# Kernel tuning notes

Measured on AMD Instinct MI355X. Metric: run time of the kernel, lower is better.

The kernel has to match this reference:

```python
import jax, jax.numpy as jnp
import numpy as np

EPS = 1e-8
NU_MOLECULAR = 1.5e-05
# loss weights (module defaults)
DATA_W, BC_W, TURB_W, RANS_W, SMOOTH_W, WALL_W = 1.0, 0.05, 0.05, 0.05, 0.01, 0.02
CONT_INIT = CONT_TGT = 0.1
MOM_INIT = MOM_TGT = 0.1
RAMP_STEPS, RAMP_START = 1000, 0

N_NODES, N_EDGES = 100000, 6400000


def _curriculum_weights(step):
    if step < RAMP_START:
        return CONT_INIT, MOM_INIT
    if step >= RAMP_START + RAMP_STEPS:
        return CONT_TGT, MOM_TGT
    alpha = (step - RAMP_START) / RAMP_STEPS  # linear ramp
    return ((1 - alpha) * CONT_INIT + alpha * CONT_TGT,
            (1 - alpha) * MOM_INIT + alpha * MOM_TGT)


def setup_inputs() -> dict:
    key = jax.random.key(0)
    k1, k2, k3, k4, k5 = jax.random.split(key, 5)
    predictions = jax.random.normal(k1, (N_NODES, 4), dtype=jnp.float32)
    targets = jax.random.normal(k2, (N_NODES, 4), dtype=jnp.float32)
    # dx, dy strictly positive edge offsets
    edge_attr_dxdy = jax.random.uniform(k3, (N_EDGES, 2), dtype=jnp.float32, minval=1e-3, maxval=0.05)
    edge_index = jax.random.randint(k4, (2, N_EDGES), 0, N_NODES, dtype=jnp.int64)
    wall_mask = jax.random.bernoulli(k5, 0.05, (N_NODES,))
    return {"predictions": predictions, "targets": targets,
            "edge_attr_dxdy": edge_attr_dxdy, "edge_index": edge_index,
            "wall_mask": wall_mask, "step": 500}


def reference(predictions, targets, edge_attr_dxdy, edge_index, wall_mask, step):
    cont_w, mom_w = _curriculum_weights(int(step))
    N = predictions.shape[0]
    row, col = edge_index[0], edge_index[1]
    u, v, p, nu_t = (predictions[:, i] for i in range(4))
    dx, dy = edge_attr_dxdy[:, 0], edge_attr_dxdy[:, 1]

    # per-edge finite differences (single gather of node fields)
    du = u[col] - u[row]
    dv = v[col] - v[row]
    dp = p[col] - p[row]

    seg = lambda e: jax.ops.segment_sum(e, row, num_segments=N)
    edge_count = jnp.maximum(seg(jnp.ones_like(du)), 1.0)

    # --- data loss ---
    mse_loss = jnp.mean((predictions - targets) ** 2)

    # --- continuity (divergence) loss ---
    divergence = (seg(du / (dx + EPS)) + seg(dv / (dy + EPS))) / edge_count
    div_loss = jnp.mean(divergence ** 2)

    # --- momentum loss ---
    p_grad_x = seg(dp / (dx + EPS)) / edge_count
    p_grad_y = seg(dp / (dy + EPS)) / edge_count
    lap_u = seg(du / (dx ** 2 + EPS)) / edge_count
    lap_v = seg(dv / (dy ** 2 + EPS)) / edge_count
    nu_eff = NU_MOLECULAR + nu_t
    momentum_loss = jnp.mean((p_grad_x + nu_eff * lap_u) ** 2 +
                             (p_grad_y + nu_eff * lap_v) ** 2)

    # --- turbulence losses ---
    positivity_loss = jnp.mean(jax.nn.relu(-nu_t) ** 2)
    du_dx = du / (dx + EPS)
    du_dy = du / (dy + EPS)
    dv_dx = dv / (dx + EPS)
    dv_dy = dv / (dy + EPS)
    strain_sq_edge = 2.0 * (du_dx ** 2 + dv_dy ** 2) + (du_dy + dv_dx) ** 2
    strain_node = seg(strain_sq_edge) / edge_count
    production = nu_t * strain_node
    turb_production_loss = jnp.mean(production ** 2)
    turb_dissipation_loss = jnp.mean(nu_t ** 2)

    # --- boundary-condition & wall-function losses (wall mask) ---
    m = wall_mask.astype(u.dtype)
    n_wall = jnp.maximum(jnp.sum(m), 1.0)
    bc_loss = jnp.sum(m * (u ** 2 + v ** 2)) / n_wall
    wall_loss = jnp.sum(m * (u ** 2 + v ** 2 + nu_t ** 2)) / n_wall

    # --- smoothness loss over edges ---
    smooth_loss = jnp.mean((predictions[col] - predictions[row]) ** 2)

    total = (DATA_W * mse_loss + cont_w * div_loss + mom_w * momentum_loss +
             TURB_W * turb_production_loss + RANS_W * turb_dissipation_loss +
             BC_W * bc_loss + SMOOTH_W * smooth_loss + WALL_W * wall_loss)
    # positivity_loss is tracked but not weighted into total (per visible code paths)
    return total
```

## Files before the change

### kernel.cpp

```cpp
#include <hip/hip_runtime.h>
#include <hip/hip_fp16.h>

#define EPS 1e-8f
#define NU_MOL 1.5e-5f
#define NPB 512
#define MAXNB 256
#define NBP 256
#define NBLK 2048
#define CMAX 3328
#define KMAX 13
#define HB 7
#define CH 1536
#define KACC 3
#define SPLIT 6
#define NGRP 32
#define GRP 64


union U32H2 { unsigned u; __half2 h; };

__device__ inline unsigned packh2(float a, float b) {
    U32H2 x; x.h = __halves2half2(__float2half_rn(a), __float2half_rn(b));
    return x.u;
}
__device__ inline float2 unpackh2(unsigned u) {
    U32H2 x; x.u = u;
    return make_float2(__low2float(x.h), __high2float(x.h));
}

__device__ inline int detect64(const void* eidx, int N) {
    const long long* ll = (const long long*)eidx;
    int is64 = 1;
    #pragma unroll
    for (int i = 0; i < 16; ++i) {
        long long v = ll[i];
        if (v < 0 || v >= (long long)N) is64 = 0;
    }
    return is64;
}


__global__ void detect_idx_dtype(const void* eidx, int N, int* flag) {
    const long long* ll = (const long long*)eidx;
    int is64 = 1;
    for (int i = 0; i < 16; ++i) {
        long long v = ll[i];
        if (v < 0 || v >= (long long)N) { is64 = 0; break; }
    }
    *flag = is64;
}

__global__ void finalize_kernel(const double* __restrict__ d,
                                const double* __restrict__ smooth_slots,
                                int N, int E, float* __restrict__ out)
{
    double smooth = 0.0;
    for (int i = 0; i < 64; ++i) smooth += smooth_slots[i];
    double dN = (double)N;
    double n_wall = d[5] > 1.0 ? d[5] : 1.0;
    double total = 1.0  * d[0] / (4.0 * dN)
                 + 0.1  * d[1] / dN
                 + 0.1  * d[2] / dN
                 + 0.05 * d[3] / dN
                 + 0.05 * d[4] / dN
                 + 0.05 * d[6] / n_wall
                 + 0.01 * smooth / (4.0 * (double)E)
                 + 0.02 * d[7] / n_wall;
    out[0] = (float)total;
}


__global__ __launch_bounds__(256) void count_kernel(
    const void* __restrict__ eidx, int E, int N, int NB,
    unsigned* __restrict__ counts, unsigned* __restrict__ gsum)
{
    __shared__ unsigned hist[4][MAXNB];
    hist[0][threadIdx.x] = 0u;
    hist[1][threadIdx.x] = 0u;
    hist[2][threadIdx.x] = 0u;
    hist[3][threadIdx.x] = 0u;
    __syncthreads();
    const int w = (threadIdx.x >> 6) & 3;
    const int is64 = detect64(eidx, N);
    const long long* ll = (const long long*)eidx;
    const int* ii = (const int*)eidx;
    int chunk = (E + NBLK - 1) / NBLK;
    int s = blockIdx.x * chunk;
    int Cb = min(chunk, E - s);

    unsigned rr[KMAX];
    #pragma unroll
    for (int k = 0; k < KMAX; ++k) {
        int i = k * 256 + threadIdx.x;
        if (i < Cb) {
            int r = is64 ? (int)ll[s + i] : ii[s + i];
            rr[k] = (unsigned)min(max(r, 0), N - 1);
        } else rr[k] = 0xFFFFFFFFu;
    }
    #pragma unroll
    for (int k = 0; k < KMAX; ++k)
        if (rr[k] != 0xFFFFFFFFu)
            atomicAdd(&hist[w][rr[k] >> 9], 1u);
    __syncthreads();
    if (threadIdx.x < NB) {
        unsigned h = hist[0][threadIdx.x] + hist[1][threadIdx.x]
                   + hist[2][threadIdx.x] + hist[3][threadIdx.x];
        counts[(size_t)blockIdx.x * NBP + threadIdx.x] = h;
        if (h) atomicAdd(&gsum[(size_t)(blockIdx.x >> 6) * NBP + threadIdx.x], h);
    }
}

__global__ __launch_bounds__(512) void scan_base_kernel(
    unsigned* __restrict__ gsum, unsigned* __restrict__ base, int NB)
{
    __shared__ unsigned sc[512];
    int t = threadIdx.x;
    unsigned vg[NGRP];
    unsigned total = 0;
    if (t < NB) {
        #pragma unroll
        for (int g = 0; g < NGRP; ++g) {
            vg[g] = gsum[(size_t)g * NBP + t];
            total += vg[g];
        }
    }
    sc[t] = total; __syncthreads();
    for (int off = 1; off < 512; off <<= 1) {
        unsigned x = (t >= off) ? sc[t - off] : 0u;
        __syncthreads();
        sc[t] += x;
        __syncthreads();
    }
    unsigned ex = sc[t] - total;
    if (t < NB) {
        base[t] = ex;
        unsigned run = ex;
        #pragma unroll
        for (int g = 0; g < NGRP; ++g) {
            unsigned x = vg[g];
            gsum[(size_t)g * NBP + t] = run;
            run += x;
        }
    }
    if (t == 511) base[NB] = sc[511];
}

__global__ __launch_bounds__(256) void local_scan_kernel(
    unsigned* __restrict__ counts, const unsigned* __restrict__ gsum, int NB)
{
    __shared__ unsigned segs[4][64];
    int g = blockIdx.x;
    int b0 = blockIdx.y * 64;
    int j = threadIdx.x & 63, seg = threadIdx.x >> 6;
    int b = b0 + j;
    unsigned v[16];
    unsigned ssum = 0;
    if (b < NB) {
        #pragma unroll
        for (int k = 0; k < 16; ++k) {
            int row = g * GRP + seg * 16 + k;
            v[k] = counts[(size_t)row * NBP + b];
            ssum += v[k];
        }
    }
    segs[seg][j] = ssum;
    __syncthreads();
    if (b < NB) {
        unsigned carry = gsum[(size_t)g * NBP + b];
        for (int s_ = 0; s_ < seg; ++s_) carry += segs[s_][j];
        #pragma unroll
        for (int k = 0; k < 16; ++k) {
            int row = g * GRP + seg * 16 + k;
            counts[(size_t)row * NBP + b] = carry;
            carry += v[k];
        }
    }
}

__global__ __launch_bounds__(256) void scatter_kernel(
    const void* __restrict__ eidx, const float2* __restrict__ eattr,
    int E, int N, int NB,
    const unsigned* __restrict__ localoff ,
    uint2* __restrict__ vals)
{
    __shared__ unsigned hist[2][MAXNB];
    __shared__ unsigned cur[MAXNB];
    __shared__ unsigned gb2[MAXNB];
    __shared__ uint2 pl[CMAX];
    __shared__ unsigned char bb[CMAX];
    __shared__ unsigned wt[4];

    const int t = threadIdx.x;
    const int blk = blockIdx.x;
    const int lane = t & 63, wv = t >> 6;
    const int w = wv & 1;
    const int is64 = detect64(eidx, N);
    const long long* ll = (const long long*)eidx;
    const int* ii = (const int*)eidx;
    const int chunk = (E + NBLK - 1) / NBLK;
    const int s = blk * chunk;
    const int Cb = min(chunk, E - s);

    hist[0][t] = 0u;
    hist[1][t] = 0u;
    __syncthreads();

    unsigned rr[KMAX], rk[KMAX];
    #pragma unroll
    for (int k = 0; k < KMAX; ++k) {
        int i = k * 256 + t;
        if (i < Cb) {
            int r = is64 ? (int)ll[s + i] : ii[s + i];
            rr[k] = (unsigned)min(max(r, 0), N - 1);
        } else rr[k] = 0xFFFFFFFFu;
    }
    #pragma unroll
    for (int k = 0; k < KMAX; ++k)
        if (rr[k] != 0xFFFFFFFFu)
            rk[k] = atomicAdd(&hist[w][rr[k] >> 9], 1u);
    if (t < NB) gb2[t] = localoff[(size_t)blk * NBP + t];
    __syncthreads();

    unsigned h = hist[0][t] + hist[1][t];
    unsigned x = h;
    #pragma unroll
    for (int off = 1; off < 64; off <<= 1) {
        unsigned y = (unsigned)__shfl_up((int)x, off, 64);
        if (lane >= off) x += y;
    }
    if (lane == 63) wt[wv] = x;
    __syncthreads();
    unsigned wadd = 0;
    for (int w2 = 0; w2 < wv; ++w2) wadd += wt[w2];
    unsigned ex = x + wadd - h;
    cur[t] = ex;
    __syncthreads();
    if (t < NB) gb2[t] -= cur[t];

    #pragma unroll
    for (int hb = 0; hb < 2; ++hb) {
        const int k0 = hb * HB;
        const int k1 = (hb == 0) ? HB : KMAX;
        int cc[HB]; float2 dd[HB];
        #pragma unroll
        for (int k = k0; k < k1; ++k) {
            int i = k * 256 + t;
            if (i < Cb) {
                int e = s + i;
                cc[k - k0] = is64 ? (int)ll[(long long)E + e] : ii[E + e];
                dd[k - k0] = eattr[e];
            }
        }
        #pragma unroll
        for (int k = k0; k < k1; ++k) {
            int i = k * 256 + t;
            if (i < Cb) {
                unsigned r = rr[k];
                unsigned b = r >> 9;
                unsigned rl = r & (NPB - 1);
                int c = min(max(cc[k - k0], 0), N - 1);
                unsigned slot = cur[b] + (w ? hist[0][b] : 0u) + rk[k];
                pl[slot] = make_uint2((unsigned)c | (rl << 17),
                                      packh2(dd[k - k0].x, dd[k - k0].y));
                bb[slot] = (unsigned char)b;
            }
        }
    }
    __syncthreads();

    #pragma unroll
    for (int hb = 0; hb < 2; ++hb) {
        const int k0 = hb * HB;
        const int k1 = (hb == 0) ? HB : KMAX;
        uint2 op[HB]; unsigned ob[HB];
        #pragma unroll
        for (int k = k0; k < k1; ++k) {
            int p = k * 256 + t;
            if (p < Cb) { op[k - k0] = pl[p]; ob[k - k0] = (unsigned)bb[p]; }
        }
        #pragma unroll
        for (int k = k0; k < k1; ++k) {
            int p = k * 256 + t;
            if (p < Cb) vals[gb2[ob[k - k0]] + (unsigned)p] = op[k - k0];
        }
    }
}

__global__ __launch_bounds__(512) void accum_kernel(
    const uint2* __restrict__ vals, const unsigned* __restrict__ base,
    const float4* __restrict__ pred, int N,
    float* __restrict__ g , double* __restrict__ smooth_slots)
{
    __shared__ float4 pl[CH];
    __shared__ uint2 ph[NPB];
    __shared__ unsigned hist[NPB];
    __shared__ unsigned cur[NPB];
    __shared__ unsigned wt[8];
    __shared__ double sm[8];

    const int b = blockIdx.x;
    const int t = threadIdx.x;
    const int wv = t >> 6, lane = t & 63;
    const int n0 = b * NPB;

    {
        int n = n0 + t;
        float4 p = (n < N) ? pred[n] : make_float4(0.f, 0.f, 0.f, 0.f);
        ph[t] = make_uint2(packh2(p.x, p.y), packh2(p.z, p.w));
    }

    unsigned s0 = base[b], e0 = base[b + 1];
    unsigned len = e0 - s0;
    unsigned s = s0 + (unsigned)(((unsigned long long)len * blockIdx.y) / SPLIT);
    unsigned e = s0 + (unsigned)(((unsigned long long)len * (blockIdx.y + 1)) / SPLIT);

    float cnt = 0, sdiv = 0, smx = 0, smy = 0, sstr = 0;
    double smooth = 0.0;

    for (unsigned cs = s; cs < e; cs += CH) {
        const int n = (int)min((unsigned)CH, e - cs);
        hist[t] = 0u;
        __syncthreads();

        uint2 vv[KACC]; unsigned rk2[KACC]; float4 pcc[KACC];
        #pragma unroll
        for (int k = 0; k < KACC; ++k) {
            int i = k * 512 + t;
            if (i < n) vv[k] = vals[cs + i];
            else vv[k].x = 0xFFFFFFFFu;
        }
        #pragma unroll
        for (int k = 0; k < KACC; ++k) {
            int i = k * 512 + t;
            if (i < n) {
                rk2[k] = atomicAdd(&hist[(vv[k].x >> 17) & (NPB - 1)], 1u);
                pcc[k] = pred[vv[k].x & 0x1FFFFu];
            }
        }
        __syncthreads();

        unsigned v = hist[t];
        unsigned x = v;
        #pragma unroll
        for (int off = 1; off < 64; off <<= 1) {
            unsigned y = (unsigned)__shfl_up((int)x, off, 64);
            if (lane >= off) x += y;
        }
        if (lane == 63) wt[wv] = x;
        __syncthreads();
        unsigned wadd = 0;
        for (int w = 0; w < wv; ++w) wadd += wt[w];
        unsigned incl = x + wadd;
        unsigned ex0 = incl - v;
        cur[t] = ex0;
        cnt += (float)v;
        __syncthreads();

        #pragma unroll
        for (int k = 0; k < KACC; ++k) {
            int i = k * 512 + t;
            if (i >= n) continue;
            unsigned pk = vv[k].x;
            unsigned rl = (pk >> 17) & (NPB - 1);
            float2 dxy = unpackh2(vv[k].y);
            float4 pc = pcc[k];
            uint2 pru = ph[rl];
            float2 pxy = unpackh2(pru.x);
            float2 pzw = unpackh2(pru.y);
            float du = pc.x - pxy.x, dv = pc.y - pxy.y;
            float dp = pc.z - pzw.x, dn = pc.w - pzw.y;
            float rx  = __builtin_amdgcn_rcpf(dxy.x + EPS);
            float ry  = __builtin_amdgcn_rcpf(dxy.y + EPS);
            float rx2 = __builtin_amdgcn_rcpf(dxy.x * dxy.x + EPS);
            float ry2 = __builtin_amdgcn_rcpf(dxy.y * dxy.y + EPS);
            float du_dx = du * rx, du_dy = du * ry;
            float dv_dx = dv * rx, dv_dy = dv * ry;
            float nu_eff = NU_MOL + pzw.y;
            float sh = du_dy + dv_dx;
            float div_e = du_dx + dv_dy;
            float mx_e  = dp * rx + nu_eff * du * rx2;
            float my_e  = dp * ry + nu_eff * dv * ry2;
            float str_e = 2.0f * (du_dx * du_dx + dv_dy * dv_dy) + sh * sh;
            pl[cur[rl] + rk2[k]] = make_float4(div_e, mx_e, my_e, str_e);
            smooth += (double)(du * du + dv * dv + dp * dp + dn * dn);
        }
        __syncthreads();

        for (unsigned i = ex0; i < incl; ++i) {
            float4 pv = pl[i];
            sdiv += pv.x;
            smx  += pv.y;
            smy  += pv.z;
            sstr += pv.w;
        }
        __syncthreads();
    }

    {
        int n = n0 + t;
        if (n < N) {
            atomicAdd(&g[0 * (size_t)N + n], cnt);
            atomicAdd(&g[1 * (size_t)N + n], sdiv);
            atomicAdd(&g[2 * (size_t)N + n], smx);
            atomicAdd(&g[3 * (size_t)N + n], smy);
            atomicAdd(&g[4 * (size_t)N + n], sstr);
        }
    }

    for (int off = 32; off > 0; off >>= 1)
        smooth += __shfl_down(smooth, off);
    if (lane == 0) sm[wv] = smooth;
    __syncthreads();
    if (t == 0) {
        double tot = 0;
        #pragma unroll
        for (int w = 0; w < 8; ++w) tot += sm[w];
        atomicAdd(&smooth_slots[(b * SPLIT + blockIdx.y) & 63], tot);
    }
}

__global__ __launch_bounds__(256) void node_final_kernel(
    const float* __restrict__ g, const float4* __restrict__ pred,
    const float4* __restrict__ tgt, const unsigned char* __restrict__ wall,
    int N, double* __restrict__ d)
{
    int i = blockIdx.x * 256 + threadIdx.x;
    double v0 = 0, v1 = 0, v2 = 0, v3 = 0, v4 = 0, v5 = 0, v6 = 0, v7 = 0;
    if (i < N) {
        float cnt = g[0 * (size_t)N + i];
        float inv = 1.0f / fmaxf(cnt, 1.0f);
        float div = g[1 * (size_t)N + i] * inv;
        float mx  = g[2 * (size_t)N + i] * inv;
        float my  = g[3 * (size_t)N + i] * inv;
        float sn  = g[4 * (size_t)N + i] * inv;
        float4 p = pred[i];
        float4 tg = tgt[i];
        float prod = p.w * sn;
        float m = wall[i] ? 1.0f : 0.0f;
        float e0 = p.x - tg.x, e1 = p.y - tg.y, e2 = p.z - tg.z, e3 = p.w - tg.w;
        float uv = p.x * p.x + p.y * p.y;
        v0 = (double)(e0 * e0 + e1 * e1 + e2 * e2 + e3 * e3);
        v1 = (double)div * (double)div;
        v2 = (double)mx * (double)mx + (double)my * (double)my;
        v3 = (double)prod * (double)prod;
        v4 = (double)p.w * (double)p.w;
        v5 = (double)m;
        v6 = (double)(m * uv);
        v7 = (double)(m * (uv + p.w * p.w));
    }
    for (int off = 32; off > 0; off >>= 1) {
        v0 += __shfl_down(v0, off); v1 += __shfl_down(v1, off);
        v2 += __shfl_down(v2, off); v3 += __shfl_down(v3, off);
        v4 += __shfl_down(v4, off); v5 += __shfl_down(v5, off);
        v6 += __shfl_down(v6, off); v7 += __shfl_down(v7, off);
    }
    __shared__ double sm[4][8];
    int lane = threadIdx.x & 63, wv = threadIdx.x >> 6;
    if (lane == 0) {
        sm[wv][0] = v0; sm[wv][1] = v1; sm[wv][2] = v2; sm[wv][3] = v3;
        sm[wv][4] = v4; sm[wv][5] = v5; sm[wv][6] = v6; sm[wv][7] = v7;
    }
    __syncthreads();
    if (threadIdx.x < 8) {
        int q = threadIdx.x;
        atomicAdd(&d[q], sm[0][q] + sm[1][q] + sm[2][q] + sm[3][q]);
    }
}


__global__ __launch_bounds__(256) void edge_kernel(
    const void* __restrict__ eidx, const float2* __restrict__ eattr,
    const float4* __restrict__ pred, int E, int N, const int* __restrict__ flag,
    float* __restrict__ a_cnt, float* __restrict__ a_div,
    float* __restrict__ a_mx, float* __restrict__ a_my,
    float* __restrict__ a_str, double* __restrict__ smooth_slots)
{
    const int is64 = *flag;
    const long long* ll = (const long long*)eidx;
    const int* ii = (const int*)eidx;
    double smooth = 0.0;
    const int stride = gridDim.x * blockDim.x;
    for (int e = blockIdx.x * blockDim.x + threadIdx.x; e < E; e += stride) {
        int row, col;
        if (is64) { row = (int)ll[e]; col = (int)ll[(long long)E + e]; }
        else      { row = ii[e];      col = ii[E + e]; }
        row = min(max(row, 0), N - 1);
        col = min(max(col, 0), N - 1);
        float2 dxy = eattr[e];
        float4 pr = pred[row];
        float4 pc = pred[col];
        float du = pc.x - pr.x, dv = pc.y - pr.y;
        float dp = pc.z - pr.z, dn = pc.w - pr.w;
        float rx  = 1.0f / (dxy.x + EPS);
        float ry  = 1.0f / (dxy.y + EPS);
        float rx2 = 1.0f / (dxy.x * dxy.x + EPS);
        float ry2 = 1.0f / (dxy.y * dxy.y + EPS);
        float du_dx = du * rx, du_dy = du * ry;
        float dv_dx = dv * rx, dv_dy = dv * ry;
        float nu_eff = NU_MOL + pr.w;
        atomicAdd(&a_cnt[row], 1.0f);
        atomicAdd(&a_div[row], du_dx + dv_dy);
        atomicAdd(&a_mx[row], dp * rx + nu_eff * du * rx2);
        atomicAdd(&a_my[row], dp * ry + nu_eff * dv * ry2);
        float sh = du_dy + dv_dx;
        atomicAdd(&a_str[row], 2.0f * (du_dx * du_dx + dv_dy * dv_dy) + sh * sh);
        smooth += (double)(du * du + dv * dv + dp * dp + dn * dn);
    }
    for (int off = 32; off > 0; off >>= 1)
        smooth += __shfl_down(smooth, off);
    __shared__ double sm[4];
    int lane = threadIdx.x & 63, wv = threadIdx.x >> 6;
    if (lane == 0) sm[wv] = smooth;
    __syncthreads();
    if (threadIdx.x == 0)
        atomicAdd(&smooth_slots[blockIdx.x & 63], sm[0] + sm[1] + sm[2] + sm[3]);
}

__global__ __launch_bounds__(256) void node_kernel(
    const float4* __restrict__ pred, const float4* __restrict__ tgt,
    const unsigned char* __restrict__ wall, int N,
    const float* __restrict__ a_cnt, const float* __restrict__ a_div,
    const float* __restrict__ a_mx, const float* __restrict__ a_my,
    const float* __restrict__ a_str, double* __restrict__ d)
{
    int i = blockIdx.x * blockDim.x + threadIdx.x;
    double v0 = 0, v1 = 0, v2 = 0, v3 = 0, v4 = 0, v5 = 0, v6 = 0, v7 = 0;
    if (i < N) {
        float4 p = pred[i];
        float4 t = tgt[i];
        float inv = 1.0f / fmaxf(a_cnt[i], 1.0f);
        float div = a_div[i] * inv;
        float mx = a_mx[i] * inv, my = a_my[i] * inv;
        float sn = a_str[i] * inv;
        float prod = p.w * sn;
        float m = wall[i] ? 1.0f : 0.0f;
        float e0 = p.x - t.x, e1 = p.y - t.y, e2 = p.z - t.z, e3 = p.w - t.w;
        float uv = p.x * p.x + p.y * p.y;
        v0 = (double)(e0 * e0 + e1 * e1 + e2 * e2 + e3 * e3);
        v1 = (double)div * (double)div;
        v2 = (double)mx * (double)mx + (double)my * (double)my;
        v3 = (double)prod * (double)prod;
        v4 = (double)p.w * (double)p.w;
        v5 = (double)m;
        v6 = (double)(m * uv);
        v7 = (double)(m * (uv + p.w * p.w));
    }
    for (int off = 32; off > 0; off >>= 1) {
        v0 += __shfl_down(v0, off); v1 += __shfl_down(v1, off);
        v2 += __shfl_down(v2, off); v3 += __shfl_down(v3, off);
        v4 += __shfl_down(v4, off); v5 += __shfl_down(v5, off);
        v6 += __shfl_down(v6, off); v7 += __shfl_down(v7, off);
    }
    __shared__ double sm[4][8];
    int lane = threadIdx.x & 63, wv = threadIdx.x >> 6;
    if (lane == 0) {
        sm[wv][0] = v0; sm[wv][1] = v1; sm[wv][2] = v2; sm[wv][3] = v3;
        sm[wv][4] = v4; sm[wv][5] = v5; sm[wv][6] = v6; sm[wv][7] = v7;
    }
    __syncthreads();
    if (threadIdx.x < 8) {
        int q = threadIdx.x;
        atomicAdd(&d[q], sm[0][q] + sm[1][q] + sm[2][q] + sm[3][q]);
    }
}


extern "C" void kernel_launch(void* const* d_in, const int* in_sizes, int n_in,
                              void* d_out, int out_size, void* d_ws, size_t ws_size,
                              hipStream_t stream) {
    const float4* pred = (const float4*)d_in[0];
    const float4* tgt  = (const float4*)d_in[1];
    const float2* eattr = (const float2*)d_in[2];
    const void* eidx = d_in[3];
    const unsigned char* wall = (const unsigned char*)d_in[4];
    int N = in_sizes[0] / 4;
    int E = in_sizes[2] / 2;
    int NB = (N + NPB - 1) / NPB;
    int chunk = (E + NBLK - 1) / NBLK;
    int ntiles = (NB + 63) / 64;

    char* ws = (char*)d_ws;
    double* d = (double*)ws;
    double* smooth_slots = d + 8;
    int* flag = (int*)(ws + 576);

    size_t off = 1024;
    float* g        = (float*)(ws + off);     off += (size_t)5 * N * 4;
    unsigned* gsum   = (unsigned*)(ws + off); off += (size_t)NGRP * NBP * 4;
    size_t zbytes = off;
    unsigned* counts = (unsigned*)(ws + off); off += (size_t)NBLK * NBP * 4;
    unsigned* base   = (unsigned*)(ws + off); off += (size_t)(NB + 1) * 4;
    off = (off + 15) & ~(size_t)15;
    uint2* vals      = (uint2*)(ws + off);    off += (size_t)E * 8;
    size_t need_fast = off;

    bool fast = (NB <= MAXNB) && (N <= 131072) && (chunk <= CMAX) &&
                (ws_size >= need_fast);

    if (fast) {
        hipMemsetAsync(d_ws, 0, zbytes, stream);
        count_kernel<<<NBLK, 256, 0, stream>>>(eidx, E, N, NB, counts, gsum);
        scan_base_kernel<<<1, 512, 0, stream>>>(gsum, base, NB);
        local_scan_kernel<<<dim3(NGRP, ntiles), 256, 0, stream>>>(counts, gsum, NB);
        scatter_kernel<<<NBLK, 256, 0, stream>>>(eidx, eattr, E, N, NB,
                                                 counts, vals);
        accum_kernel<<<dim3(NB, SPLIT), 512, 0, stream>>>(vals, base, pred, N,
                                                          g, smooth_slots);
        node_final_kernel<<<(N + 255) / 256, 256, 0, stream>>>(g, pred, tgt, wall,
                                                               N, d);
        finalize_kernel<<<1, 1, 0, stream>>>(d, smooth_slots, N, E, (float*)d_out);
    } else {
        float* arrays = (float*)(ws + 1024);
        float* a_cnt = arrays + (size_t)0 * N;
        float* a_div = arrays + (size_t)1 * N;
        float* a_mx  = arrays + (size_t)2 * N;
        float* a_my  = arrays + (size_t)3 * N;
        float* a_str = arrays + (size_t)4 * N;
        size_t zb = 1024 + (size_t)5 * N * sizeof(float);
        hipMemsetAsync(d_ws, 0, zb, stream);
        detect_idx_dtype<<<1, 1, 0, stream>>>(eidx, N, flag);
        edge_kernel<<<4096, 256, 0, stream>>>(eidx, eattr, pred, E, N, flag,
                                              a_cnt, a_div, a_mx, a_my, a_str,
                                              smooth_slots);
        node_kernel<<<(N + 255) / 256, 256, 0, stream>>>(pred, tgt, wall, N,
                                                         a_cnt, a_div, a_mx, a_my,
                                                         a_str, d);
        finalize_kernel<<<1, 1, 0, stream>>>(d, smooth_slots, N, E, (float*)d_out);
    }
}
```

Measured before the change: 227.0 us.

## Replace histogram-scan-scatter accumulation with LDS float atomics per node

The per-chunk histogram, prefix scan, scatter into a shared staging buffer and serial per-node reduction are replaced by five shared-memory float atomic adds per edge into per-node accumulators. This removes three block barriers per chunk and the serial per-thread reduction loop, and enlarges the chunk to 2048 edges. In exchange each edge issues five LDS atomics that may contend on hot rows, and summation order becomes nondeterministic.

```diff
diff --git a/kernel.cpp b/kernel.cpp
--- a/kernel.cpp
+++ b/kernel.cpp
@@ -10,8 +10,6 @@
 #define CMAX 3328
 #define KMAX 13
 #define HB 7
-#define CH 1536
-#define KACC 3
 #define SPLIT 6
 #define NGRP 32
 #define GRP 64
@@ -291,11 +289,8 @@
     const float4* __restrict__ pred, int N,
     float* __restrict__ g , double* __restrict__ smooth_slots)
 {
-    __shared__ float4 pl[CH];
+    __shared__ float acc0[NPB], acc1[NPB], acc2[NPB], acc3[NPB], acc4[NPB];
     __shared__ uint2 ph[NPB];
-    __shared__ unsigned hist[NPB];
-    __shared__ unsigned cur[NPB];
-    __shared__ unsigned wt[8];
     __shared__ double sm[8];
 
     const int b = blockIdx.x;
@@ -307,57 +302,34 @@
         int n = n0 + t;
         float4 p = (n < N) ? pred[n] : make_float4(0.f, 0.f, 0.f, 0.f);
         ph[t] = make_uint2(packh2(p.x, p.y), packh2(p.z, p.w));
-    }
+        acc0[t] = 0.f; acc1[t] = 0.f; acc2[t] = 0.f;
+        acc3[t] = 0.f; acc4[t] = 0.f;
+    }
+    __syncthreads();
 
     unsigned s0 = base[b], e0 = base[b + 1];
     unsigned len = e0 - s0;
     unsigned s = s0 + (unsigned)(((unsigned long long)len * blockIdx.y) / SPLIT);
     unsigned e = s0 + (unsigned)(((unsigned long long)len * (blockIdx.y + 1)) / SPLIT);
 
-    float cnt = 0, sdiv = 0, smx = 0, smy = 0, sstr = 0;
     double smooth = 0.0;
 
-    for (unsigned cs = s; cs < e; cs += CH) {
-        const int n = (int)min((unsigned)CH, e - cs);
-        hist[t] = 0u;
-        __syncthreads();
-
-        uint2 vv[KACC]; unsigned rk2[KACC]; float4 pcc[KACC];
-        #pragma unroll
-        for (int k = 0; k < KACC; ++k) {
+    for (unsigned cs = s; cs < e; cs += 4 * 512) {
+        const int n = (int)min((unsigned)(4 * 512), e - cs);
+        uint2 vv[4]; float4 pcc[4];
+        #pragma unroll
+        for (int k = 0; k < 4; ++k) {
             int i = k * 512 + t;
             if (i < n) vv[k] = vals[cs + i];
             else vv[k].x = 0xFFFFFFFFu;
         }
         #pragma unroll
-        for (int k = 0; k < KACC; ++k) {
+        for (int k = 0; k < 4; ++k) {
             int i = k * 512 + t;
-            if (i < n) {
-                rk2[k] = atomicAdd(&hist[(vv[k].x >> 17) & (NPB - 1)], 1u);
-                pcc[k] = pred[vv[k].x & 0x1FFFFu];
-            }
-        }
-        __syncthreads();
-
-        unsigned v = hist[t];
-        unsigned x = v;
-        #pragma unroll
-        for (int off = 1; off < 64; off <<= 1) {
-            unsigned y = (unsigned)__shfl_up((int)x, off, 64);
-            if (lane >= off) x += y;
-        }
-        if (lane == 63) wt[wv] = x;
-        __syncthreads();
-        unsigned wadd = 0;
-        for (int w = 0; w < wv; ++w) wadd += wt[w];
-        unsigned incl = x + wadd;
-        unsigned ex0 = incl - v;
-        cur[t] = ex0;
-        cnt += (float)v;
-        __syncthreads();
-
-        #pragma unroll
-        for (int k = 0; k < KACC; ++k) {
+            if (i < n) pcc[k] = pred[vv[k].x & 0x1FFFFu];
+        }
+        #pragma unroll
+        for (int k = 0; k < 4; ++k) {
             int i = k * 512 + t;
             if (i >= n) continue;
             unsigned pk = vv[k].x;
@@ -381,29 +353,24 @@
             float mx_e  = dp * rx + nu_eff * du * rx2;
             float my_e  = dp * ry + nu_eff * dv * ry2;
             float str_e = 2.0f * (du_dx * du_dx + dv_dy * dv_dy) + sh * sh;
-            pl[cur[rl] + rk2[k]] = make_float4(div_e, mx_e, my_e, str_e);
+            unsafeAtomicAdd(&acc0[rl], 1.0f);
+            unsafeAtomicAdd(&acc1[rl], div_e);
+            unsafeAtomicAdd(&acc2[rl], mx_e);
+            unsafeAtomicAdd(&acc3[rl], my_e);
+            unsafeAtomicAdd(&acc4[rl], str_e);
             smooth += (double)(du * du + dv * dv + dp * dp + dn * dn);
         }
-        __syncthreads();
-
-        for (unsigned i = ex0; i < incl; ++i) {
-            float4 pv = pl[i];
-            sdiv += pv.x;
-            smx  += pv.y;
-            smy  += pv.z;
-            sstr += pv.w;
-        }
-        __syncthreads();
-    }
+    }
+    __syncthreads();
 
     {
         int n = n0 + t;
         if (n < N) {
-            atomicAdd(&g[0 * (size_t)N + n], cnt);
-            atomicAdd(&g[1 * (size_t)N + n], sdiv);
-            atomicAdd(&g[2 * (size_t)N + n], smx);
-            atomicAdd(&g[3 * (size_t)N + n], smy);
-            atomicAdd(&g[4 * (size_t)N + n], sstr);
+            atomicAdd(&g[0 * (size_t)N + n], acc0[t]);
+            atomicAdd(&g[1 * (size_t)N + n], acc1[t]);
+            atomicAdd(&g[2 * (size_t)N + n], acc2[t]);
+            atomicAdd(&g[3 * (size_t)N + n], acc3[t]);
+            atomicAdd(&g[4 * (size_t)N + n], acc4[t]);
         }
     }
 
```

After: 374.7 us. +65.1%, slower.

## Fuse global and local count scans and halve sort block count

Applied to the files above, without the earlier changes.

Merges the single-block base scan and the per-group local scan into one kernel. Each block recomputes the global bucket prefix from the group sums, so one launch and a serial single-block step disappear. Zeroing of the node accumulator array moves from the memset into this kernel, which shrinks the memset. Counting and scatter now use half as many blocks, each handling twice as many edges with more register-staged items per thread. This cuts the counts matrix and the group count, at the cost of higher per-block shared memory and register pressure and less parallelism.

```diff
diff --git a/kernel.cpp b/kernel.cpp
--- a/kernel.cpp
+++ b/kernel.cpp
@@ -6,14 +6,15 @@
 #define NPB 512
 #define MAXNB 256
 #define NBP 256
-#define NBLK 2048
-#define CMAX 3328
-#define KMAX 13
-#define HB 7
+#define NBLK 1024
+#define CMAX 6400
+#define HB 5
+#define NHB 5
+#define KMAX 25
 #define CH 1536
 #define KACC 3
 #define SPLIT 6
-#define NGRP 32
+#define NGRP 16
 #define GRP 64
 
 
@@ -110,55 +111,64 @@
     }
 }
 
-__global__ __launch_bounds__(512) void scan_base_kernel(
-    unsigned* __restrict__ gsum, unsigned* __restrict__ base, int NB)
-{
-    __shared__ unsigned sc[512];
-    int t = threadIdx.x;
+__global__ __launch_bounds__(256) void scanlocal_kernel(
+    unsigned* __restrict__ counts, const unsigned* __restrict__ gsum,
+    unsigned* __restrict__ base, float* __restrict__ g, int N, int NB)
+{
+    __shared__ unsigned runstart[NBP];
+    __shared__ unsigned segs[4][64];
+    __shared__ unsigned wt[4];
+
+    const int t = threadIdx.x;
+    const int gidx = blockIdx.x;
+    const int lane = t & 63, wv = t >> 6;
+
     unsigned vg[NGRP];
-    unsigned total = 0;
-    if (t < NB) {
-        #pragma unroll
-        for (int g = 0; g < NGRP; ++g) {
-            vg[g] = gsum[(size_t)g * NBP + t];
-            total += vg[g];
-        }
-    }
-    sc[t] = total; __syncthreads();
-    for (int off = 1; off < 512; off <<= 1) {
-        unsigned x = (t >= off) ? sc[t - off] : 0u;
-        __syncthreads();
-        sc[t] += x;
-        __syncthreads();
-    }
-    unsigned ex = sc[t] - total;
-    if (t < NB) {
-        base[t] = ex;
-        unsigned run = ex;
-        #pragma unroll
-        for (int g = 0; g < NGRP; ++g) {
-            unsigned x = vg[g];
-            gsum[(size_t)g * NBP + t] = run;
-            run += x;
-        }
-    }
-    if (t == 511) base[NB] = sc[511];
-}
-
-__global__ __launch_bounds__(256) void local_scan_kernel(
-    unsigned* __restrict__ counts, const unsigned* __restrict__ gsum, int NB)
-{
-    __shared__ unsigned segs[4][64];
-    int g = blockIdx.x;
+    unsigned total = 0, pref = 0;
+    #pragma unroll
+    for (int q = 0; q < NGRP; ++q) {
+        vg[q] = gsum[(size_t)q * NBP + t];
+        if (q < gidx) pref += vg[q];
+        total += vg[q];
+    }
+    unsigned x = total;
+    #pragma unroll
+    for (int off = 1; off < 64; off <<= 1) {
+        unsigned y = (unsigned)__shfl_up((int)x, off, 64);
+        if (lane >= off) x += y;
+    }
+    if (lane == 63) wt[wv] = x;
+    __syncthreads();
+    unsigned wadd = 0;
+    for (int w2 = 0; w2 < wv; ++w2) wadd += wt[w2];
+    unsigned incl = x + wadd;
+    unsigned ex = incl - total;
+    runstart[t] = ex + pref;
+    if (gidx == 0 && blockIdx.y == 0) {
+        if (t < NB) base[t] = ex;
+        if (t == 255) base[NB] = incl;
+    }
+    __syncthreads();
+
+    {
+        size_t totf = (size_t)5 * N;
+        int nblk = gridDim.x * gridDim.y;
+        int bid = blockIdx.y * gridDim.x + blockIdx.x;
+        size_t per = (totf + nblk - 1) / nblk;
+        size_t s0 = (size_t)bid * per;
+        size_t e0 = s0 + per; if (e0 > totf) e0 = totf;
+        for (size_t i = s0 + t; i < e0; i += 256) g[i] = 0.f;
+    }
+
     int b0 = blockIdx.y * 64;
-    int j = threadIdx.x & 63, seg = threadIdx.x >> 6;
+    int j = t & 63, seg = t >> 6;
     int b = b0 + j;
     unsigned v[16];
     unsigned ssum = 0;
     if (b < NB) {
         #pragma unroll
         for (int k = 0; k < 16; ++k) {
-            int row = g * GRP + seg * 16 + k;
+            int row = gidx * GRP + seg * 16 + k;
             v[k] = counts[(size_t)row * NBP + b];
             ssum += v[k];
         }
@@ -166,11 +176,11 @@
     segs[seg][j] = ssum;
     __syncthreads();
     if (b < NB) {
-        unsigned carry = gsum[(size_t)g * NBP + b];
+        unsigned carry = runstart[b];
         for (int s_ = 0; s_ < seg; ++s_) carry += segs[s_][j];
         #pragma unroll
         for (int k = 0; k < 16; ++k) {
-            int row = g * GRP + seg * 16 + k;
+            int row = gidx * GRP + seg * 16 + k;
             counts[(size_t)row * NBP + b] = carry;
             carry += v[k];
         }
@@ -238,12 +248,11 @@
     if (t < NB) gb2[t] -= cur[t];
 
     #pragma unroll
-    for (int hb = 0; hb < 2; ++hb) {
+    for (int hb = 0; hb < NHB; ++hb) {
         const int k0 = hb * HB;
-        const int k1 = (hb == 0) ? HB : KMAX;
         int cc[HB]; float2 dd[HB];
         #pragma unroll
-        for (int k = k0; k < k1; ++k) {
+        for (int k = k0; k < k0 + HB; ++k) {
             int i = k * 256 + t;
             if (i < Cb) {
                 int e = s + i;
@@ -252,7 +261,7 @@
             }
         }
         #pragma unroll
-        for (int k = k0; k < k1; ++k) {
+        for (int k = k0; k < k0 + HB; ++k) {
             int i = k * 256 + t;
             if (i < Cb) {
                 unsigned r = rr[k];
@@ -269,17 +278,16 @@
     __syncthreads();
 
     #pragma unroll
-    for (int hb = 0; hb < 2; ++hb) {
+    for (int hb = 0; hb < NHB; ++hb) {
         const int k0 = hb * HB;
-        const int k1 = (hb == 0) ? HB : KMAX;
         uint2 op[HB]; unsigned ob[HB];
         #pragma unroll
-        for (int k = k0; k < k1; ++k) {
+        for (int k = k0; k < k0 + HB; ++k) {
             int p = k * 256 + t;
             if (p < Cb) { op[k - k0] = pl[p]; ob[k - k0] = (unsigned)bb[p]; }
         }
         #pragma unroll
-        for (int k = k0; k < k1; ++k) {
+        for (int k = k0; k < k0 + HB; ++k) {
             int p = k * 256 + t;
             if (p < Cb) vals[gb2[ob[k - k0]] + (unsigned)p] = op[k - k0];
         }
@@ -585,9 +593,9 @@
     int* flag = (int*)(ws + 576);
 
     size_t off = 1024;
-    float* g        = (float*)(ws + off);     off += (size_t)5 * N * 4;
     unsigned* gsum   = (unsigned*)(ws + off); off += (size_t)NGRP * NBP * 4;
     size_t zbytes = off;
+    float* g        = (float*)(ws + off);     off += (size_t)5 * N * 4;
     unsigned* counts = (unsigned*)(ws + off); off += (size_t)NBLK * NBP * 4;
     unsigned* base   = (unsigned*)(ws + off); off += (size_t)(NB + 1) * 4;
     off = (off + 15) & ~(size_t)15;
@@ -600,8 +608,8 @@
     if (fast) {
         hipMemsetAsync(d_ws, 0, zbytes, stream);
         count_kernel<<<NBLK, 256, 0, stream>>>(eidx, E, N, NB, counts, gsum);
-        scan_base_kernel<<<1, 512, 0, stream>>>(gsum, base, NB);
-        local_scan_kernel<<<dim3(NGRP, ntiles), 256, 0, stream>>>(counts, gsum, NB);
+        scanlocal_kernel<<<dim3(NGRP, ntiles), 256, 0, stream>>>(counts, gsum,
+                                                                 base, g, N, NB);
         scatter_kernel<<<NBLK, 256, 0, stream>>>(eidx, eattr, E, N, NB,
                                                  counts, vals);
         accum_kernel<<<dim3(NB, SPLIT), 512, 0, stream>>>(vals, base, pred, N,
```

Result: slower. 234.1 us (+3.1%).
